# Kernel tuning notes

Hardware: AMD Instinct MI355X
Metric: run time of the kernel (lower is better)

Reference implementation:

```python
import jax, jax.numpy as jnp
import numpy as np

B, N, M, D, H, K, V = 2, 2048, 2048, 1024, 16, 64, 64
MAX_WAVELENGTH = 10000
SCALE_FACTOR = 1.0


def rope(x, positions, max_wavelength, scale_factor):
    # x: [b, s, h, k]; positions: [b, s] int
    head_dim = x.shape[-1]
    fraction = 2.0 * jnp.arange(head_dim // 2, dtype=x.dtype) / head_dim
    timescale = jnp.asarray(max_wavelength, x.dtype) ** fraction            # [k/2]
    # scaled positions -> phase per (b, s, 1 head bcast, k/2)
    phase = (positions.astype(x.dtype) / scale_factor)[:, :, None, None] / timescale  # [b,s,1,k/2]
    sin, cos = jnp.sin(phase), jnp.cos(phase)
    x1, x2 = jnp.split(x, 2, axis=-1)
    return jnp.concatenate([x1 * cos - x2 * sin, x2 * cos + x1 * sin], axis=-1)


def setup_inputs() -> dict:
    key = jax.random.key(0)
    ks = jax.random.split(key, 8)
    scale = 1.0 / np.sqrt(D)  # keep logits numerically sane with random params
    inp = {
        "query": jax.random.normal(ks[0], (B, N, D), jnp.float32),
        "q_positions": jnp.broadcast_to(jnp.arange(N, dtype=jnp.int32), (B, N)),
        "key": jax.random.normal(ks[1], (B, M, D), jnp.float32),
        "k_positions": jnp.broadcast_to(jnp.arange(M, dtype=jnp.int32), (B, M)),
        "value": jax.random.normal(ks[2], (B, M, D), jnp.float32),
        "mask": jnp.ones((1, 1, N, M), dtype=bool),
        "P_q": jax.random.normal(ks[3], (H, D, K), jnp.float32) * scale,
        "P_k": jax.random.normal(ks[4], (H, D, K), jnp.float32) * scale,
        "P_v": jax.random.normal(ks[5], (H, D, V), jnp.float32) * scale,
        "P_o": jax.random.normal(ks[6], (H, D, V), jnp.float32) * scale,
    }
    return inp


def reference(query, q_positions, key, k_positions, value, mask, P_q, P_k, P_v, P_o):
    q = jnp.einsum('bnd,hdk->bnhk', query, P_q)
    k = jnp.einsum('bmd,hdk->bmhk', key, P_k)
    v = jnp.einsum('bmd,hdv->bmhv', value, P_v)
    q = rope(q, q_positions, MAX_WAVELENGTH, SCALE_FACTOR)
    k = rope(k, k_positions, MAX_WAVELENGTH, SCALE_FACTOR)
    logits = jnp.einsum('bnhk,bmhk->bhnm', q, k)
    if mask is not None:
        logits = jnp.where(mask, logits, -jnp.inf)
    weights = jax.nn.softmax(logits, axis=-1)
    o = jnp.einsum('bhnm,bmhv->bnhv', weights, v)
    return jnp.einsum('bnhv,hdv->bnd', o, P_o)
```

## Files before the change

kernel.cpp:

```cpp
#include <hip/hip_runtime.h>
#include <hip/hip_bf16.h>
#include <math.h>

#define B_ 2
#define N_ 2048
#define M_ 2048
#define D_ 1024
#define H_ 16


typedef _Float16 f16;
typedef f16  f16x2 __attribute__((ext_vector_type(2)));
typedef f16  f16x4 __attribute__((ext_vector_type(4)));
typedef f16  f16x8 __attribute__((ext_vector_type(8)));
typedef float f32x4  __attribute__((ext_vector_type(4)));
typedef float f32x16 __attribute__((ext_vector_type(16)));

#define MFMA16(a, b, c) __builtin_amdgcn_mfma_f32_16x16x32_f16((a), (b), (c), 0, 0, 0)
#define MFMA32(a, b, c) __builtin_amdgcn_mfma_f32_32x32x16_f16((a), (b), (c), 0, 0, 0)
#define LDST 72
#define EXP2(x) __builtin_amdgcn_exp2f(x)

#define GLOAD_LDS(g, l)                                             \
  __builtin_amdgcn_global_load_lds(                                 \
      (const __attribute__((address_space(1))) void*)(g),           \
      (__attribute__((address_space(3))) void*)(l), 16, 0, 0)

static __device__ __forceinline__ unsigned int pk2(float a, float b) {
  auto h = __builtin_amdgcn_cvt_pkrtz(a, b);
  return __builtin_bit_cast(unsigned int, h);
}
static __device__ __forceinline__ float max3f(float a, float b, float c) {
  return fmaxf(fmaxf(a, b), c);
}

__global__ __launch_bounds__(256) void prep_all(
    const float* __restrict__ Pq, const float* __restrict__ Pk,
    const float* __restrict__ Pv, const float* __restrict__ Po,
    const int* __restrict__ qpos, const int* __restrict__ kpos,
    const float* __restrict__ Aq, const float* __restrict__ Ak,
    const float* __restrict__ Av,
    f16* __restrict__ Ptq, f16* __restrict__ Ptk, f16* __restrict__ Ptv,
    f16* __restrict__ Wo, float2* __restrict__ tabq, float2* __restrict__ tabk,
    f16* __restrict__ A16q, f16* __restrict__ A16k, f16* __restrict__ A16v)
{
  __shared__ float Ts[64][65];
  const int z = blockIdx.y, x = blockIdx.x, tid = threadIdx.x;
  if (z < 3) {
    if (x >= 256) return;
    const float* P = (z == 0) ? Pq : (z == 1) ? Pk : Pv;
    f16* Pt = (z == 0) ? Ptq : (z == 1) ? Ptk : Ptv;
    const int d0 = (x & 15) * 64, h = x >> 4;
    #pragma unroll
    for (int it = 0; it < 4; ++it) {
      int fi = tid + 256 * it;
      int dr = fi >> 4, c4 = (fi & 15) << 2;
      float4 v = *(const float4*)(P + ((size_t)h * D_ + d0 + dr) * 64 + c4);
      Ts[dr][c4+0] = v.x; Ts[dr][c4+1] = v.y; Ts[dr][c4+2] = v.z; Ts[dr][c4+3] = v.w;
    }
    __syncthreads();
    const int c = tid >> 2, dp = (tid & 3) * 16;
    f16x8 w0, w1;
    #pragma unroll
    for (int i = 0; i < 8; ++i) { w0[i] = (f16)Ts[dp + i][c]; w1[i] = (f16)Ts[dp + 8 + i][c]; }
    f16* dst = Pt + ((size_t)h * 64 + c) * D_ + d0 + dp;
    *(f16x8*)dst = w0;
    *(f16x8*)(dst + 8) = w1;
  } else if (z == 3) {
    int e = (x * 256 + tid) * 4;
    if (e >= H_ * D_ * 64) return;
    int h = e >> 16, d = (e >> 6) & 1023, v = e & 63;
    float4 xx = *(const float4*)(Po + e);
    f16x4 w = {(f16)xx.x, (f16)xx.y, (f16)xx.z, (f16)xx.w};
    *(f16x4*)&Wo[(size_t)d * 1024 + h * 64 + v] = w;
  } else if (z < 6) {
    if (x >= 512) return;
    int idx = x * 256 + tid;
    int r = idx >> 5, c = idx & 31;
    const int* pos = (z == 4) ? qpos : kpos;
    float2* tab = (z == 4) ? tabq : tabk;
    float fpos = (float)pos[r];
    float inv_ts = exp2f(-(float)c * 0.4152410118609203f);
    float ph = fpos * inv_ts, sn, cs;
    sincosf(ph, &sn, &cs);
    tab[idx] = make_float2(cs, sn);
  } else {
    const float* s = (z == 6) ? Aq : (z == 7) ? Ak : Av;
    f16* d = (z == 6) ? A16q : (z == 7) ? A16k : A16v;
    size_t e = ((size_t)x * 256 + tid) * 16;
    #pragma unroll
    for (int half = 0; half < 2; ++half) {
      float4 v0 = *(const float4*)(s + e + half * 8);
      float4 v1 = *(const float4*)(s + e + half * 8 + 4);
      f16x8 w = {(f16)v0.x, (f16)v0.y, (f16)v0.z, (f16)v0.w,
                 (f16)v1.x, (f16)v1.y, (f16)v1.z, (f16)v1.w};
      *(f16x8*)(d + e + half * 8) = w;
    }
  }
}

__global__ __launch_bounds__(256) void gemm_fused(
    const f16* __restrict__ Aq, const f16* __restrict__ Ak,
    const f16* __restrict__ Av,
    const f16* __restrict__ Bq, const f16* __restrict__ Bk,
    const f16* __restrict__ Bv,
    const float2* __restrict__ tabq, const float2* __restrict__ tabk,
    f16* __restrict__ dq, f16* __restrict__ dk, f16* __restrict__ dv)
{
  __shared__ f16 As[2][128 * 64];
  __shared__ f16 Bs[2][128 * 64];
  const int tid = threadIdx.x, lane = tid & 63, wave = tid >> 6;
  const int quad = lane >> 4, l16 = lane & 15;
  const int lb = blockIdx.x + 8 * (int)blockIdx.y;
  const int xcd = lb & 7, t = lb >> 3;
  const int col0 = (t & 7) * 128;
  const int row0 = (xcd * 4 + (t >> 3)) * 128;
  const int op = blockIdx.z;
  const int wr = (wave >> 1) * 64, wc = (wave & 1) * 64;

  const f16* A  = (op == 0) ? Aq : (op == 1) ? Ak : Av;
  const f16* Bt = (op == 0) ? Bq : (op == 1) ? Bk : Bv;

  f32x4 acc[4][4] = {};
  const int srow = wave * 8 + (lane >> 3);
  const int scol = ((lane & 7) ^ ((lane >> 3) & 7)) * 8;
  const int sdst = wave * 512 + lane * 8;
  const int rx   = l16 & 7;

#define STAGE_F(b, kk)                                                       \
  _Pragma("unroll")                                                          \
  for (int c = 0; c < 4; ++c) {                                              \
    GLOAD_LDS(A  + (size_t)(row0 + c * 32 + srow) * 1024 + (kk) + scol,      \
              &As[b][c * 2048 + sdst]);                                      \
    GLOAD_LDS(Bt + (size_t)(col0 + c * 32 + srow) * 1024 + (kk) + scol,      \
              &Bs[b][c * 2048 + sdst]);                                      \
  }

#define COMPUTE_F(b)                                                         \
  _Pragma("unroll")                                                          \
  for (int ks = 0; ks < 2; ++ks) {                                           \
    f16x8 af[4], bf[4];                                                      \
    _Pragma("unroll")                                                        \
    for (int i = 0; i < 4; ++i)                                              \
      af[i] = *(const f16x8*)&As[b][(wr + i * 16 + l16) * 64 +               \
                                    ((ks * 4 + quad) ^ rx) * 8];             \
    _Pragma("unroll")                                                        \
    for (int j = 0; j < 4; ++j)                                              \
      bf[j] = *(const f16x8*)&Bs[b][(wc + j * 16 + l16) * 64 +               \
                                    ((ks * 4 + quad) ^ rx) * 8];             \
    __builtin_amdgcn_s_setprio(1);                                           \
    _Pragma("unroll")                                                        \
    for (int i = 0; i < 4; ++i)                                              \
      _Pragma("unroll")                                                      \
      for (int j = 0; j < 4; ++j)                                            \
        acc[i][j] = MFMA16(af[i], bf[j], acc[i][j]);                         \
    __builtin_amdgcn_s_setprio(0);                                           \
  }

  STAGE_F(0, 0);
  __syncthreads();
  for (int k0 = 0; k0 < 1024; k0 += 128) {
    STAGE_F(1, k0 + 64);
    COMPUTE_F(0);
    __syncthreads();
    if (k0 + 128 < 1024) STAGE_F(0, k0 + 128);
    COMPUTE_F(1);
    __syncthreads();
  }
#undef STAGE_F
#undef COMPUTE_F

  if (op == 2) {
    #pragma unroll
    for (int i = 0; i < 4; ++i) {
      int r = row0 + wr + i * 16 + quad * 4;
      int b = r >> 11, s = r & 2047;
      #pragma unroll
      for (int j = 0; j < 4; ++j) {
        int col = col0 + wc + j * 16 + l16;
        int h = col >> 6, v = col & 63;
        f16x4 w = {(f16)acc[i][j][0], (f16)acc[i][j][1],
                   (f16)acc[i][j][2], (f16)acc[i][j][3]};
        *(f16x4*)&dv[((size_t)(b * H_ + h) * 64 + v) * 2048 + s] = w;
      }
    }
  } else {
    const float2* tab = (op == 0) ? tabq : tabk;
    f16* oq = (op == 0) ? dq : dk;
    const float qs = (op == 0) ? 1.4426950408889634f : 1.0f;
    #pragma unroll
    for (int i = 0; i < 4; ++i) {
      #pragma unroll
      for (int reg = 0; reg < 4; ++reg) {
        int r = row0 + wr + i * 16 + quad * 4 + reg;
        int b = r >> 11, s = r & 2047;
        #pragma unroll
        for (int j = 0; j < 2; ++j) {
          int col = col0 + wc + j * 16 + l16;
          int h = col >> 6, c = col & 63;
          float2 cs = tab[r * 32 + c];
          float x1 = acc[i][j][reg], x2 = acc[i][j + 2][reg];
          size_t base = ((size_t)(b * H_ + h) * 2048 + s) * 64;
          oq[base + c]      = (f16)((x1 * cs.x - x2 * cs.y) * qs);
          oq[base + c + 32] = (f16)((x2 * cs.x + x1 * cs.y) * qs);
        }
      }
    }
  }
}

__global__ __launch_bounds__(512, 4) void flash7e(
    const f16* __restrict__ q, const f16* __restrict__ k,
    const f16* __restrict__ vt, f16* __restrict__ o)
{
  __shared__ __align__(16) char smem[4 * 64 * LDST * sizeof(f16)];

  const int tid = threadIdx.x, lane = tid & 63, wave = tid >> 6;
  const int g = wave >> 2, w4 = wave & 3;
  const int L = lane >> 5, nl = lane & 31;
  const int lin = blockIdx.x + 16 * (blockIdx.y + 16 * (int)blockIdx.z);
  const int xcd = lin & 7, t = lin >> 3;
  const int hb = xcd * 4 + (t >> 4);
  const int n0 = (t & 15) * 128;
  const int h = hb & 15, b = hb >> 4;

  f16* Ks  = (f16*)smem + (size_t)g * (64 * LDST);
  f16* Vts = (f16*)smem + (size_t)(2 + g) * (64 * LDST);

  const f16* qb = q  + (size_t)(b * H_ + h) * N_ * 64;
  const f16* kb = k  + (size_t)(b * H_ + h) * M_ * 64 + (size_t)g * 1024 * 64;
  const f16* vb = vt + (size_t)(b * H_ + h) * 64 * M_ + g * 1024;

  f16x8 qf[4];
  #pragma unroll
  for (int gg = 0; gg < 4; ++gg)
    qf[gg] = *(const f16x8*)(qb + (size_t)(n0 + w4 * 32 + nl) * 64 + gg * 16 + L * 8);

  f32x16 acc[2] = {};
  float mst = -INFINITY;
  float lst = 0.f;

  const int gtid = tid & 255;
  const int srow = gtid >> 2, soff = (gtid & 3) * 16;

  f16x8 kp0 = *(const f16x8*)(kb + (size_t)srow * 64 + soff);
  f16x8 kp1 = *(const f16x8*)(kb + (size_t)srow * 64 + soff + 8);
  f16x8 vp0 = *(const f16x8*)(vb + (size_t)srow * M_ + soff);
  f16x8 vp1 = *(const f16x8*)(vb + (size_t)srow * M_ + soff + 8);

  for (int m0 = 0; m0 < 1024; m0 += 64) {
    __syncthreads();
    *(f16x8*)&Ks[srow * LDST + soff]      = kp0;
    *(f16x8*)&Ks[srow * LDST + soff + 8]  = kp1;
    *(f16x8*)&Vts[srow * LDST + soff]     = vp0;
    *(f16x8*)&Vts[srow * LDST + soff + 8] = vp1;
    __syncthreads();
    if (m0 + 64 < 1024) {
      kp0 = *(const f16x8*)(kb + (size_t)(m0 + 64 + srow) * 64 + soff);
      kp1 = *(const f16x8*)(kb + (size_t)(m0 + 64 + srow) * 64 + soff + 8);
      vp0 = *(const f16x8*)(vb + (size_t)srow * M_ + m0 + 64 + soff);
      vp1 = *(const f16x8*)(vb + (size_t)srow * M_ + m0 + 64 + soff + 8);
    }

    f32x16 s[2] = {};
    __builtin_amdgcn_s_setprio(1);
    #pragma unroll
    for (int u = 0; u < 2; ++u)
      #pragma unroll
      for (int gg = 0; gg < 4; ++gg) {
        f16x8 af = *(const f16x8*)&Ks[(u * 32 + nl) * LDST + gg * 16 + L * 8];
        s[u] = MFMA32(af, qf[gg], s[u]);
      }
    __builtin_amdgcn_s_setprio(0);

    float a11[11];
    #pragma unroll
    for (int i = 0; i < 10; ++i) {
      int j = 3 * i;
      float x0 = (j < 16) ? s[0][j] : s[1][j - 16];
      float x1 = (j + 1 < 16) ? s[0][j + 1] : s[1][j - 15];
      float x2 = (j + 2 < 16) ? s[0][j + 2] : s[1][j - 14];
      a11[i] = max3f(x0, x1, x2);
    }
    a11[10] = fmaxf(s[1][14], s[1][15]);
    float b4_0 = max3f(a11[0], a11[1], a11[2]);
    float b4_1 = max3f(a11[3], a11[4], a11[5]);
    float b4_2 = max3f(a11[6], a11[7], a11[8]);
    float b4_3 = fmaxf(a11[9], a11[10]);
    float mx = fmaxf(fmaxf(b4_0, b4_1), fmaxf(b4_2, b4_3));
    mx = fmaxf(mx, __shfl_xor(mx, 32));
    float m_new = fmaxf(mst, mx);

    if (!__all(mx - mst <= 8.0f)) {
      float alpha = EXP2(mst - m_new);
      #pragma unroll
      for (int u = 0; u < 2; ++u)
        #pragma unroll
        for (int r = 0; r < 16; ++r) acc[u][r] *= alpha;
      lst *= alpha;
      mst = m_new;
    }

    #pragma unroll
    for (int u = 0; u < 2; ++u)
      #pragma unroll
      for (int r = 0; r < 16; ++r)
        s[u][r] = EXP2(s[u][r] - mst);

    unsigned int qw[2][4][2];
    #pragma unroll
    for (int u = 0; u < 2; ++u)
      #pragma unroll
      for (int rq = 0; rq < 4; ++rq) {
        qw[u][rq][0] = pk2(s[u][rq * 4 + 0], s[u][rq * 4 + 1]);
        qw[u][rq][1] = pk2(s[u][rq * 4 + 2], s[u][rq * 4 + 3]);
      }

#if __has_builtin(__builtin_amdgcn_fdot2)
    {
      const f16x2 one2 = {(f16)1.0f, (f16)1.0f};
      float sum = 0.f;
      #pragma unroll
      for (int u = 0; u < 2; ++u)
        #pragma unroll
        for (int rq = 0; rq < 4; ++rq)
          #pragma unroll
          for (int w = 0; w < 2; ++w)
            sum = __builtin_amdgcn_fdot2(
                __builtin_bit_cast(f16x2, qw[u][rq][w]), one2, sum, false);
      sum += __shfl_xor(sum, 32);
      lst += sum;
    }
#else
    {
      float ts[16];
      #pragma unroll
      for (int r = 0; r < 16; ++r) ts[r] = s[0][r] + s[1][r];
      #pragma unroll
      for (int st = 8; st >= 1; st >>= 1)
        #pragma unroll
        for (int r = 0; r < st; ++r) ts[r] += ts[r + st];
      float sum = ts[0];
      sum += __shfl_xor(sum, 32);
      lst += sum;
    }
#endif

    union PBu { unsigned int w[4]; f16x8 v; } pb[4];
    #pragma unroll
    for (int u = 0; u < 2; ++u)
      #pragma unroll
      for (int gg = 0; gg < 2; ++gg)
        #pragma unroll
        for (int w = 0; w < 2; ++w) {
          unsigned int a = qw[u][2 * gg][w], bb = qw[u][2 * gg + 1][w];
          asm volatile("v_permlane32_swap_b32 %0, %1" : "+v"(a), "+v"(bb));
          pb[2 * u + gg].w[w]     = a;
          pb[2 * u + gg].w[2 + w] = bb;
        }

    __builtin_amdgcn_s_setprio(1);
    #pragma unroll
    for (int u = 0; u < 2; ++u)
      #pragma unroll
      for (int gg = 0; gg < 4; ++gg) {
        f16x8 vf = *(const f16x8*)&Vts[(u * 32 + nl) * LDST + gg * 16 + L * 8];
        acc[u] = MFMA32(vf, pb[gg].v, acc[u]);
      }
    __builtin_amdgcn_s_setprio(0);
  }

  float* mrg = (float*)smem;
  const int mb = (w4 * 64 + lane) * 34;
  __syncthreads();
  if (g == 1) {
    #pragma unroll
    for (int r = 0; r < 16; ++r) { mrg[mb + r] = acc[0][r]; mrg[mb + 16 + r] = acc[1][r]; }
    mrg[mb + 32] = mst;
    mrg[mb + 33] = lst;
  }
  __syncthreads();
  if (g == 0) {
    float m1 = mrg[mb + 32], l1 = mrg[mb + 33];
    float Mm = fmaxf(mst, m1);
    float a0 = EXP2(mst - Mm), a1 = EXP2(m1 - Mm);
    float invl = 1.0f / (a0 * lst + a1 * l1);
    f16* ob = o + ((size_t)(b * N_ + n0 + w4 * 32 + nl) * 1024) + h * 64;
    #pragma unroll
    for (int u = 0; u < 2; ++u)
      #pragma unroll
      for (int rq = 0; rq < 4; ++rq) {
        f16x4 w;
        #pragma unroll
        for (int j = 0; j < 4; ++j)
          w[j] = (f16)((a0 * acc[u][rq * 4 + j] + a1 * mrg[mb + u * 16 + rq * 4 + j]) * invl);
        *(f16x4*)&ob[u * 32 + 8 * rq + 4 * L] = w;
      }
  }
}

__global__ __launch_bounds__(256) void gemm_out(
    const f16* __restrict__ A, const f16* __restrict__ Bt,
    float* __restrict__ out)
{
  __shared__ f16 As[2][128 * 64];
  __shared__ f16 Bs[2][64 * 64];
  const int tid = threadIdx.x, lane = tid & 63, wave = tid >> 6;
  const int quad = lane >> 4, l16 = lane & 15;
  const int lb = blockIdx.x + 16 * (int)blockIdx.y;
  const int xcd = lb & 7, t = lb >> 3;
  const int col0 = (t & 15) * 64;
  const int row0 = (xcd * 4 + (t >> 4)) * 128;
  const int wr = (wave >> 1) * 64, wc = (wave & 1) * 32;

  f32x4 acc[4][2] = {};
  const int srow = wave * 8 + (lane >> 3);
  const int scol = ((lane & 7) ^ ((lane >> 3) & 7)) * 8;
  const int sdst = wave * 512 + lane * 8;
  const int rx   = l16 & 7;

#define STAGE_O(b, kk)                                                       \
  _Pragma("unroll")                                                          \
  for (int c = 0; c < 4; ++c)                                                \
    GLOAD_LDS(A + (size_t)(row0 + c * 32 + srow) * 1024 + (kk) + scol,       \
              &As[b][c * 2048 + sdst]);                                      \
  _Pragma("unroll")                                                          \
  for (int c = 0; c < 2; ++c)                                                \
    GLOAD_LDS(Bt + (size_t)(col0 + c * 32 + srow) * 1024 + (kk) + scol,      \
              &Bs[b][c * 2048 + sdst]);

#define COMPUTE_O(b)                                                         \
  _Pragma("unroll")                                                          \
  for (int ks = 0; ks < 2; ++ks) {                                           \
    f16x8 af[4], bf[2];                                                      \
    _Pragma("unroll")                                                        \
    for (int i = 0; i < 4; ++i)                                              \
      af[i] = *(const f16x8*)&As[b][(wr + i * 16 + l16) * 64 +               \
                                    ((ks * 4 + quad) ^ rx) * 8];             \
    _Pragma("unroll")                                                        \
    for (int j = 0; j < 2; ++j)                                              \
      bf[j] = *(const f16x8*)&Bs[b][(wc + j * 16 + l16) * 64 +               \
                                    ((ks * 4 + quad) ^ rx) * 8];             \
    __builtin_amdgcn_s_setprio(1);                                           \
    _Pragma("unroll")                                                        \
    for (int i = 0; i < 4; ++i)                                              \
      _Pragma("unroll")                                                      \
      for (int j = 0; j < 2; ++j)                                            \
        acc[i][j] = MFMA16(af[i], bf[j], acc[i][j]);                         \
    __builtin_amdgcn_s_setprio(0);                                           \
  }

  STAGE_O(0, 0);
  __syncthreads();
  for (int k0 = 0; k0 < 1024; k0 += 128) {
    STAGE_O(1, k0 + 64);
    COMPUTE_O(0);
    __syncthreads();
    if (k0 + 128 < 1024) STAGE_O(0, k0 + 128);
    COMPUTE_O(1);
    __syncthreads();
  }
#undef STAGE_O
#undef COMPUTE_O

  #pragma unroll
  for (int i = 0; i < 4; ++i)
    #pragma unroll
    for (int j = 0; j < 2; ++j)
      #pragma unroll
      for (int reg = 0; reg < 4; ++reg)
        out[(size_t)(row0 + wr + i * 16 + quad * 4 + reg) * 1024 +
            col0 + wc + j * 16 + l16] = acc[i][j][reg];
}

extern "C" void kernel_launch(void* const* d_in, const int* in_sizes, int n_in,
                              void* d_out, int out_size, void* d_ws, size_t ws_size,
                              hipStream_t stream) {
  (void)in_sizes; (void)n_in; (void)out_size; (void)ws_size;
  const float* query = (const float*)d_in[0];
  const int*   qpos  = (const int*)d_in[1];
  const float* key   = (const float*)d_in[2];
  const int*   kpos  = (const int*)d_in[3];
  const float* value = (const float*)d_in[4];
  const float* Pq = (const float*)d_in[6];
  const float* Pk = (const float*)d_in[7];
  const float* Pv = (const float*)d_in[8];
  const float* Po = (const float*)d_in[9];
  float* out = (float*)d_out;

  const size_t pm = (size_t)1024 * 1024;
  const size_t em = (size_t)B_ * H_ * 2048 * 64;
  f16* Ptq = (f16*)d_ws;
  f16* Ptk = Ptq + pm;
  f16* Ptv = Ptk + pm;
  f16* Wo  = Ptv + pm;
  f16* q_ws  = Wo + pm;
  f16* k_ws  = q_ws + em;
  f16* vt_ws = k_ws + em;
  f16* o_ws  = vt_ws + em;
  float2* tabq = (float2*)(o_ws + em);
  float2* tabk = tabq + (size_t)4096 * 32;
  f16* a16q = (f16*)(tabk + (size_t)4096 * 32);
  f16* a16k = a16q + em;
  f16* a16v = a16k + em;

  dim3 blk(256);
  prep_all<<<dim3(1024, 9), blk, 0, stream>>>(
      Pq, Pk, Pv, Po, qpos, kpos, query, key, value,
      Ptq, Ptk, Ptv, Wo, tabq, tabk, a16q, a16k, a16v);

  gemm_fused<<<dim3(8, 32, 3), blk, 0, stream>>>(
      a16q, a16k, a16v, Ptq, Ptk, Ptv, tabq, tabk, q_ws, k_ws, vt_ws);

  flash7e<<<dim3(N_ / 128, H_, B_), dim3(512), 0, stream>>>(q_ws, k_ws, vt_ws, o_ws);

  gemm_out<<<dim3(16, 32), blk, 0, stream>>>(o_ws, Wo, out);
}
```

Before: 225.2 us.

## Double-buffer K/V tiles in LDS with one barrier per iteration

The flash attention kernel now keeps two LDS buffers for the K and V^T tiles. The next tile is written into the alternate buffer midway through the current iteration, so each iteration needs one __syncthreads instead of two. The goal is to hide the LDS store and barrier cost behind the softmax and MFMA work. It doubles LDS use to about 73 KB per block, which may lower how many blocks fit per CU compared with the launch bound of 4.

```diff
diff --git a/kernel.cpp b/kernel.cpp
--- a/kernel.cpp
+++ b/kernel.cpp
@@ -209,11 +209,11 @@
   }
 }
 
-__global__ __launch_bounds__(512, 4) void flash7e(
+__global__ __launch_bounds__(512, 4) void flash7f(
     const f16* __restrict__ q, const f16* __restrict__ k,
     const f16* __restrict__ vt, f16* __restrict__ o)
 {
-  __shared__ __align__(16) char smem[4 * 64 * LDST * sizeof(f16)];
+  __shared__ __align__(16) char smem[8 * 64 * LDST * sizeof(f16)];
 
   const int tid = threadIdx.x, lane = tid & 63, wave = tid >> 6;
   const int g = wave >> 2, w4 = wave & 3;
@@ -224,8 +224,8 @@
   const int n0 = (t & 15) * 128;
   const int h = hb & 15, b = hb >> 4;
 
-  f16* Ks  = (f16*)smem + (size_t)g * (64 * LDST);
-  f16* Vts = (f16*)smem + (size_t)(2 + g) * (64 * LDST);
+  f16* base = (f16*)smem;
+  const int REG = 64 * LDST;
 
   const f16* qb = q  + (size_t)(b * H_ + h) * N_ * 64;
   const f16* kb = k  + (size_t)(b * H_ + h) * M_ * 64 + (size_t)g * 1024 * 64;
@@ -247,15 +247,23 @@
   f16x8 kp1 = *(const f16x8*)(kb + (size_t)srow * 64 + soff + 8);
   f16x8 vp0 = *(const f16x8*)(vb + (size_t)srow * M_ + soff);
   f16x8 vp1 = *(const f16x8*)(vb + (size_t)srow * M_ + soff + 8);
-
-  for (int m0 = 0; m0 < 1024; m0 += 64) {
-    __syncthreads();
-    *(f16x8*)&Ks[srow * LDST + soff]      = kp0;
-    *(f16x8*)&Ks[srow * LDST + soff + 8]  = kp1;
-    *(f16x8*)&Vts[srow * LDST + soff]     = vp0;
-    *(f16x8*)&Vts[srow * LDST + soff + 8] = vp1;
-    __syncthreads();
-    if (m0 + 64 < 1024) {
+  {
+    f16* Ksw  = base + g * REG;
+    f16* Vtsw = base + (4 + g) * REG;
+    *(f16x8*)&Ksw[srow * LDST + soff]      = kp0;
+    *(f16x8*)&Ksw[srow * LDST + soff + 8]  = kp1;
+    *(f16x8*)&Vtsw[srow * LDST + soff]     = vp0;
+    *(f16x8*)&Vtsw[srow * LDST + soff + 8] = vp1;
+  }
+  __syncthreads();
+
+  for (int tt = 0; tt < 16; ++tt) {
+    const int cur = tt & 1;
+    const int m0 = tt * 64;
+    f16* Ksr  = base + (cur * 2 + g) * REG;
+    f16* Vtsr = base + (4 + cur * 2 + g) * REG;
+
+    if (tt < 15) {
       kp0 = *(const f16x8*)(kb + (size_t)(m0 + 64 + srow) * 64 + soff);
       kp1 = *(const f16x8*)(kb + (size_t)(m0 + 64 + srow) * 64 + soff + 8);
       vp0 = *(const f16x8*)(vb + (size_t)srow * M_ + m0 + 64 + soff);
@@ -268,7 +276,7 @@
     for (int u = 0; u < 2; ++u)
       #pragma unroll
       for (int gg = 0; gg < 4; ++gg) {
-        f16x8 af = *(const f16x8*)&Ks[(u * 32 + nl) * LDST + gg * 16 + L * 8];
+        f16x8 af = *(const f16x8*)&Ksr[(u * 32 + nl) * LDST + gg * 16 + L * 8];
         s[u] = MFMA32(af, qf[gg], s[u]);
       }
     __builtin_amdgcn_s_setprio(0);
@@ -306,6 +314,15 @@
       #pragma unroll
       for (int r = 0; r < 16; ++r)
         s[u][r] = EXP2(s[u][r] - mst);
+
+    if (tt < 15) {
+      f16* Ksw  = base + ((cur ^ 1) * 2 + g) * REG;
+      f16* Vtsw = base + (4 + (cur ^ 1) * 2 + g) * REG;
+      *(f16x8*)&Ksw[srow * LDST + soff]      = kp0;
+      *(f16x8*)&Ksw[srow * LDST + soff + 8]  = kp1;
+      *(f16x8*)&Vtsw[srow * LDST + soff]     = vp0;
+      *(f16x8*)&Vtsw[srow * LDST + soff + 8] = vp1;
+    }
 
     unsigned int qw[2][4][2];
     #pragma unroll
@@ -364,15 +381,16 @@
     for (int u = 0; u < 2; ++u)
       #pragma unroll
       for (int gg = 0; gg < 4; ++gg) {
-        f16x8 vf = *(const f16x8*)&Vts[(u * 32 + nl) * LDST + gg * 16 + L * 8];
+        f16x8 vf = *(const f16x8*)&Vtsr[(u * 32 + nl) * LDST + gg * 16 + L * 8];
         acc[u] = MFMA32(vf, pb[gg].v, acc[u]);
       }
     __builtin_amdgcn_s_setprio(0);
+
+    __syncthreads();
   }
 
   float* mrg = (float*)smem;
   const int mb = (w4 * 64 + lane) * 34;
-  __syncthreads();
   if (g == 1) {
     #pragma unroll
     for (int r = 0; r < 16; ++r) { mrg[mb + r] = acc[0][r]; mrg[mb + 16 + r] = acc[1][r]; }
@@ -512,7 +530,7 @@
   gemm_fused<<<dim3(8, 32, 3), blk, 0, stream>>>(
       a16q, a16k, a16v, Ptq, Ptk, Ptv, tabq, tabk, q_ws, k_ws, vt_ws);
 
-  flash7e<<<dim3(N_ / 128, H_, B_), dim3(512), 0, stream>>>(q_ws, k_ws, vt_ws, o_ws);
+  flash7f<<<dim3(N_ / 128, H_, B_), dim3(512), 0, stream>>>(q_ws, k_ws, vt_ws, o_ws);
 
   gemm_out<<<dim3(16, 32), blk, 0, stream>>>(o_ws, Wo, out);
 }
```

After: 231.6 us. 2.8% more time.
